# Performance work log

Hardware: AMD Instinct MI355X
Metric: run time of the kernel (lower is better)

## Reference

```python
import jax, jax.numpy as jnp
import numpy as np

D = 1024      # embedding_size
H = 16        # num_heads
HD = D // H   # head_size
EPS = 1e-5


def setup_inputs() -> dict:
    key = jax.random.key(0)
    ks = jax.random.split(key, 12)
    s_in = 1.0 / np.sqrt(D)
    s_hid = 1.0 / np.sqrt(4 * D)
    return {
        "x": jax.random.normal(ks[0], (2, 2048, D), dtype=jnp.float32),
        # per-head projections, no bias: [H, D, HD]
        "Wq": jax.random.normal(ks[1], (H, D, HD), dtype=jnp.float32) * s_in,
        "Wk": jax.random.normal(ks[2], (H, D, HD), dtype=jnp.float32) * s_in,
        "Wv": jax.random.normal(ks[3], (H, D, HD), dtype=jnp.float32) * s_in,
        "Wo": jax.random.normal(ks[4], (D, D), dtype=jnp.float32) * s_in,
        "bo": jnp.zeros((D,), dtype=jnp.float32),
        "W1": jax.random.normal(ks[5], (D, 4 * D), dtype=jnp.float32) * s_in,
        "b1": jnp.zeros((4 * D,), dtype=jnp.float32),
        "W2": jax.random.normal(ks[6], (4 * D, D), dtype=jnp.float32) * s_hid,
        "b2": jnp.zeros((D,), dtype=jnp.float32),
        "g1": jnp.ones((D,), dtype=jnp.float32),
        "be1": jnp.zeros((D,), dtype=jnp.float32),
        "g2": jnp.ones((D,), dtype=jnp.float32),
        "be2": jnp.zeros((D,), dtype=jnp.float32),
    }


def _layernorm(x, g, b):
    mu = jnp.mean(x, axis=-1, keepdims=True)
    var = jnp.mean(jnp.square(x - mu), axis=-1, keepdims=True)
    return (x - mu) * jax.lax.rsqrt(var + EPS) * g + b


def _block(x, Wq, Wk, Wv, Wo, bo, W1, b1, W2, b2, g1, be1, g2, be2):
    B, T, _ = x.shape
    h = _layernorm(x, g1, be1)
    # per-head projections: [B, H, T, HD]
    q = jnp.einsum('btd,hde->bhte', h, Wq)
    k = jnp.einsum('btd,hde->bhte', h, Wk)
    v = jnp.einsum('btd,hde->bhte', h, Wv)
    # NOTE: original scales by embedding_size**-0.5 (x.shape[-1]), not head_size
    scores = jnp.einsum('bhte,bhse->bhts', q, k) * (D ** -0.5)
    mask = jnp.tril(jnp.ones((T, T), dtype=bool))
    scores = jnp.where(mask, scores, -jnp.inf)
    attn = jax.nn.softmax(scores, axis=-1)           # dropout = identity (eval)
    out = jnp.einsum('bhts,bhse->bhte', attn, v)      # [B, H, T, HD]
    out = out.transpose(0, 2, 1, 3).reshape(B, T, D)  # concat heads
    x = x + (out @ Wo + bo)
    h2 = _layernorm(x, g2, be2)
    ffn = jax.nn.relu(h2 @ W1 + b1) @ W2 + b2
    return x + ffn


def reference(x, Wq, Wk, Wv, Wo, bo, W1, b1, W2, b2, g1, be1, g2, be2):
    return _block(x, Wq, Wk, Wv, Wo, bo, W1, b1, W2, b2, g1, be1, g2, be2)
```

## Files before the change

### kernel.cpp

```cpp
#include <hip/hip_runtime.h>
#include <stdint.h>

typedef unsigned short u16;
typedef __attribute__((ext_vector_type(8))) __bf16 bf16x8;
typedef __attribute__((ext_vector_type(4))) float f32x4;

#define D_EMB 1024
#define NHEAD 16
#define HDIM 64
#define TSEQ 2048
#define NTOK 4096
#define NEG_BIG -1.0e30f

#define GLD16(lp, gp) __builtin_amdgcn_global_load_lds( \
    (const __attribute__((address_space(1))) unsigned int*)(gp), \
    (__attribute__((address_space(3))) unsigned int*)(lp), 16, 0, 0)

__device__ __forceinline__ float bf2f(u16 u) {
    union { unsigned int i; float f; } c; c.i = ((unsigned int)u) << 16; return c.f;
}
__device__ __forceinline__ u16 f2bf(float f) {
    union { float f; unsigned int i; } c; c.f = f;
    unsigned int r = (c.i + 0x7FFFu + ((c.i >> 16) & 1u)) >> 16;
    return (u16)r;
}
__device__ __forceinline__ void cp16(u16* dst, const u16* src) {
    *reinterpret_cast<uint4*>(dst) = *reinterpret_cast<const uint4*>(src);
}
__device__ __forceinline__ float load_in(const u16* p, size_t idx, int f32) {
    return f32 ? reinterpret_cast<const float*>(p)[idx] : bf2f(p[idx]);
}
__device__ __forceinline__ size_t tidx(int row, int col, int KB) {
    int c = (col & 7) | ((((col >> 3) ^ row) & 3) << 3);
    return ((size_t)((row >> 7) * KB + (col >> 5)) * 128 + (row & 127)) * 32 + c;
}

__global__ void detect_kernel(const u16* __restrict__ x, u16* __restrict__ fl) {
    if (threadIdx.x == 0) {
        int f = 0;
        for (int i = 0; i < 128; ++i) {
            float v = fabsf(bf2f(x[i]));
            if (!(v <= 1.0e3f)) f = 1;
        }
        fl[0] = (u16)f;
    }
}

__global__ __launch_bounds__(256) void transpose_tiled_kernel(
        const u16* __restrict__ X, u16* __restrict__ Xt, int KB,
        const u16* __restrict__ fl) {
    __shared__ __align__(16) u16 Ts[64 * 72];
    int f32 = fl[0];
    int bi = blockIdx.y, bj = blockIdx.x;
    int NS = gridDim.x * 64;
    int t = threadIdx.x;
    for (int p = 0; p < 2; ++p) {
        int idx = p * 256 + t;
        int row = idx >> 3, col8 = (idx & 7) * 8;
        size_t src = (size_t)(bi * 64 + row) * NS + bj * 64 + col8;
        if (f32) {
            for (int jj = 0; jj < 8; ++jj)
                Ts[row * 72 + col8 + jj] = f2bf(reinterpret_cast<const float*>(X)[src + jj]);
        } else {
            cp16(&Ts[row * 72 + col8], &X[src]);
        }
    }
    __syncthreads();
    for (int p = 0; p < 2; ++p) {
        int idx = p * 256 + t;
        int row = idx >> 3, col8 = (idx & 7) * 8;
        union { u16 u[8]; uint4 v; } tmp;
        for (int jj = 0; jj < 8; ++jj) tmp.u[jj] = Ts[(col8 + jj) * 72 + row];
        int n = bj * 64 + row, k0 = bi * 64 + col8;
        *reinterpret_cast<uint4*>(&Xt[tidx(n, k0, KB)]) = tmp.v;
    }
}

__global__ __launch_bounds__(256) void pack_qkv_kernel(
        const u16* __restrict__ Wq, const u16* __restrict__ Wk,
        const u16* __restrict__ Wv, u16* __restrict__ Wt,
        const u16* __restrict__ fl) {
    int f32 = fl[0];
    int idx = blockIdx.x * 256 + threadIdx.x;
    int e = idx & 63, d8 = (idx >> 6) & 127, hh = (idx >> 13) & 15, sel = idx >> 17;
    const u16* W = (sel == 0) ? Wq : ((sel == 1) ? Wk : Wv);
    int n = sel * 1024 + hh * 64 + e;
    size_t src = (size_t)hh * (D_EMB * HDIM) + (size_t)(d8 * 8) * HDIM + e;
    union { u16 u[8]; uint4 v; } tmp;
    for (int dd = 0; dd < 8; ++dd) {
        float v = f32 ? reinterpret_cast<const float*>(W)[src + (size_t)dd * HDIM]
                      : bf2f(W[src + (size_t)dd * HDIM]);
        tmp.u[dd] = f2bf(v);
    }
    *reinterpret_cast<uint4*>(&Wt[tidx(n, d8 * 8, 32)]) = tmp.v;
}

__global__ __launch_bounds__(256) void ln_kernel(
        const u16* __restrict__ X, const u16* __restrict__ g,
        const u16* __restrict__ be, u16* __restrict__ Ht,
        const u16* __restrict__ fl) {
    int f32 = fl[0];
    int row = blockIdx.x;
    int t = threadIdx.x;
    float v[4];
    float s = 0.f, sq = 0.f;
    for (int i = 0; i < 4; ++i) {
        v[i] = load_in(X, (size_t)row * D_EMB + t + i * 256, f32);
        s += v[i]; sq += v[i] * v[i];
    }
    for (int m = 32; m; m >>= 1) { s += __shfl_down(s, m); sq += __shfl_down(sq, m); }
    __shared__ float red[8];
    int wid = t >> 6, lane = t & 63;
    if (lane == 0) { red[wid] = s; red[wid + 4] = sq; }
    __syncthreads();
    if (t == 0) {
        float S = red[0] + red[1] + red[2] + red[3];
        float SQ = red[4] + red[5] + red[6] + red[7];
        float mean = S * (1.f / 1024.f);
        float var = SQ * (1.f / 1024.f) - mean * mean;
        red[0] = mean; red[1] = rsqrtf(var + 1e-5f);
    }
    __syncthreads();
    float mean = red[0], rstd = red[1];
    for (int i = 0; i < 4; ++i) {
        int c = t + i * 256;
        float hv = (v[i] - mean) * rstd * load_in(g, c, f32) + load_in(be, c, f32);
        Ht[tidx(row, c, 32)] = f2bf(hv);
    }
}

template<int TAG, int TN>
__global__ __launch_bounds__(256) void gemm_t(
        const u16* __restrict__ At, const u16* __restrict__ Bt, u16* __restrict__ C,
        u16* __restrict__ C2,
        const u16* __restrict__ bias, const u16* __restrict__ res,
        int N, int K, int flags, int row_off,
        const u16* __restrict__ fl) {
    constexpr int NF = (TN == 128) ? 4 : 2;
    __shared__ __align__(16) u16 As2[2][4096];
    __shared__ __align__(16) u16 Bs2[2][TN * 32];
    int f32 = fl[0];
    int t = threadIdx.x;
    int gx = gridDim.x, gy = gridDim.y;
    int id = blockIdx.y * gx + blockIdx.x;
    int total = gx * gy;
    int xcd = id & 7, seq = id >> 3, P = total >> 3;
    int tpb = (P >= 32) ? 32 : 16;
    int th  = (P >= 32) ? 8 : 4;
    int tile = xcd * (P / tpb) + seq / tpb;
    int within = seq % tpb;
    int tiles_x = gx >> 2;
    int bx = (tile % tiles_x) * 4 + (within & 3);
    int by = (tile / tiles_x) * th + (within >> 2);
    int n0 = bx * TN, m0 = by * 128;
    int w = t >> 6, lane = t & 63, quad = lane >> 4, l16 = lane & 15;
    int wm = (TN == 128) ? (w >> 1) * 64 : (w & 1) * 64;
    int wn = (TN == 128) ? (w & 1) * 64  : (w >> 1) * 32;
    int KB = K >> 5;
    int kb0 = (seq * (KB >> 5)) & (KB - 1);
    const u16* Ab = At + (size_t)(m0 >> 7) * KB * 4096 + w * 512 + lane * 8;
    const u16* Bb = Bt + (size_t)(n0 >> 7) * KB * 4096
                       + ((TN == 64) ? (n0 & 64) * 32 : 0) + w * 512 + lane * 8;

    auto stage = [&](int buf, int kb) {
        const u16* ga = Ab + (size_t)kb * 4096;
        const u16* gb = Bb + (size_t)kb * 4096;
        u16* la = &As2[buf][w * 512];
        u16* lb = &Bs2[buf][w * 512];
        GLD16(la, ga);
        GLD16(la + 2048, ga + 2048);
        GLD16(lb, gb);
        if constexpr (TN == 128) { GLD16(lb + 2048, gb + 2048); }
    };

    const f32x4 fz = {0.f, 0.f, 0.f, 0.f};
    f32x4 acc[4][NF];
    for (int mt = 0; mt < 4; ++mt)
        for (int nt = 0; nt < NF; ++nt) acc[mt][nt] = fz;

    stage(0, kb0);
    __syncthreads();
    int kb = kb0;
    for (int it = 0; it < KB; ++it) {
        int cur = it & 1;
        int kn = (kb + 1 == KB) ? 0 : kb + 1;
        if (it + 1 < KB) stage(cur ^ 1, kn);
        bf16x8 af[4], bfr[NF];
        for (int mt = 0; mt < 4; ++mt) {
            int r = wm + mt * 16 + l16;
            af[mt] = *reinterpret_cast<const bf16x8*>(
                &As2[cur][r * 32 + (((quad ^ r) & 3) << 3)]);
        }
        for (int nt = 0; nt < NF; ++nt) {
            int r = wn + nt * 16 + l16;
            bfr[nt] = *reinterpret_cast<const bf16x8*>(
                &Bs2[cur][r * 32 + (((quad ^ r) & 3) << 3)]);
        }
        for (int mt = 0; mt < 4; ++mt)
            for (int nt = 0; nt < NF; ++nt)
                acc[mt][nt] = __builtin_amdgcn_mfma_f32_16x16x32_bf16(af[mt], bfr[nt], acc[mt][nt], 0, 0, 0);
        __syncthreads();
        kb = kn;
    }

    int relu_f = flags & 1, out_ext = flags & 2, c_tiled = flags & 4, qkvsp = flags & 8;
    if (qkvsp) {
        for (int mt = 0; mt < 4; ++mt)
            for (int nt = 0; nt < NF; ++nt) {
                int gc = n0 + wn + nt * 16 + l16;
                int grb = m0 + wm + mt * 16 + quad * 4;
                if (gc < 2048) {
                    for (int r = 0; r < 4; ++r)
                        C[(size_t)(grb + r) * 2048 + gc] = f2bf(acc[mt][nt][r]);
                } else {
                    int hh = (gc - 2048) >> 6, d = gc & 63;
                    int bb = grb >> 11, s = grb & 2047;
                    union { u16 u[4]; uint2 v; } pk;
                    for (int r = 0; r < 4; ++r) pk.u[r] = f2bf(acc[mt][nt][r]);
                    *reinterpret_cast<uint2*>(
                        &C2[(((size_t)bb * 16 + hh) * 64 + d) * 2048 + s]) = pk.v;
                }
            }
        return;
    }
    for (int mt = 0; mt < 4; ++mt)
        for (int nt = 0; nt < NF; ++nt)
            for (int r = 0; r < 4; ++r) {
                int gr = m0 + wm + mt * 16 + quad * 4 + r;
                int gc = n0 + wn + nt * 16 + l16;
                float v = acc[mt][nt][r];
                if (bias) v += load_in(bias, gc, f32);
                if (relu_f) v = v > 0.f ? v : 0.f;
                size_t oidx = (size_t)(row_off + gr) * N + gc;
                if (res) v += load_in(res, oidx, f32);
                if (c_tiled)      C[tidx(gr, gc, N >> 5)] = f2bf(v);
                else if (out_ext && f32) reinterpret_cast<float*>(C)[oidx] = v;
                else              C[oidx] = f2bf(v);
            }
}

template<int TAG, int KBL, int TN>
__global__ __launch_bounds__(256) void gemm_sk_t(
        const u16* __restrict__ At, const u16* __restrict__ Bt,
        float* __restrict__ Pp, int N, int K) {
    constexpr int NF = (TN == 128) ? 4 : 2;
    __shared__ __align__(16) u16 As2[2][4096];
    __shared__ __align__(16) u16 Bs2[2][TN * 32];
    int t = threadIdx.x;
    int gx = gridDim.x, gy = gridDim.y;
    int id = blockIdx.y * gx + blockIdx.x;
    int total = gx * gy;
    int xcd = id & 7, seq = id >> 3, P = total >> 3;
    int tpb = (P >= 32) ? 32 : 16;
    int th  = (P >= 32) ? 8 : 4;
    int tile = xcd * (P / tpb) + seq / tpb;
    int within = seq % tpb;
    int tiles_x = gx >> 2;
    int bx = (tile % tiles_x) * 4 + (within & 3);
    int by = (tile / tiles_x) * th + (within >> 2);
    int n0 = bx * TN, m0 = by * 128;
    int w = t >> 6, lane = t & 63, quad = lane >> 4, l16 = lane & 15;
    int wm = (TN == 128) ? (w >> 1) * 64 : (w & 1) * 64;
    int wn = (TN == 128) ? (w & 1) * 64  : (w >> 1) * 32;
    int KB = K >> 5;
    int kstart = blockIdx.z * KBL;
    int rel0 = seq & (KBL - 1);
    const u16* Ab = At + (size_t)(m0 >> 7) * KB * 4096 + w * 512 + lane * 8;
    const u16* Bb = Bt + (size_t)(n0 >> 7) * KB * 4096
                       + ((TN == 64) ? (n0 & 64) * 32 : 0) + w * 512 + lane * 8;

    auto stage = [&](int buf, int kb) {
        const u16* ga = Ab + (size_t)kb * 4096;
        const u16* gb = Bb + (size_t)kb * 4096;
        u16* la = &As2[buf][w * 512];
        u16* lb = &Bs2[buf][w * 512];
        GLD16(la, ga);
        GLD16(la + 2048, ga + 2048);
        GLD16(lb, gb);
        if constexpr (TN == 128) { GLD16(lb + 2048, gb + 2048); }
    };

    const f32x4 fz = {0.f, 0.f, 0.f, 0.f};
    f32x4 acc[4][NF];
    for (int mt = 0; mt < 4; ++mt)
        for (int nt = 0; nt < NF; ++nt) acc[mt][nt] = fz;

    stage(0, kstart + rel0);
    __syncthreads();
    for (int it = 0; it < KBL; ++it) {
        int cur = it & 1;
        if (it + 1 < KBL)
            stage(cur ^ 1, kstart + ((rel0 + it + 1) & (KBL - 1)));
        bf16x8 af[4], bfr[NF];
        for (int mt = 0; mt < 4; ++mt) {
            int r = wm + mt * 16 + l16;
            af[mt] = *reinterpret_cast<const bf16x8*>(
                &As2[cur][r * 32 + (((quad ^ r) & 3) << 3)]);
        }
        for (int nt = 0; nt < NF; ++nt) {
            int r = wn + nt * 16 + l16;
            bfr[nt] = *reinterpret_cast<const bf16x8*>(
                &Bs2[cur][r * 32 + (((quad ^ r) & 3) << 3)]);
        }
        for (int mt = 0; mt < 4; ++mt)
            for (int nt = 0; nt < NF; ++nt)
                acc[mt][nt] = __builtin_amdgcn_mfma_f32_16x16x32_bf16(af[mt], bfr[nt], acc[mt][nt], 0, 0, 0);
        __syncthreads();
    }

    for (int mt = 0; mt < 4; ++mt)
        for (int nt = 0; nt < NF; ++nt)
            for (int r = 0; r < 4; ++r) {
                int gr = m0 + wm + mt * 16 + quad * 4 + r;
                int gc = n0 + wn + nt * 16 + l16;
                atomicAdd(&Pp[(size_t)gr * N + gc], acc[mt][nt][r]);
            }
}

__global__ __launch_bounds__(256) void zero_f32_kernel(float* __restrict__ p) {
    const f32x4 fz = {0.f, 0.f, 0.f, 0.f};
    reinterpret_cast<f32x4*>(p)[(size_t)blockIdx.x * 256 + threadIdx.x] = fz;
}

__global__ __launch_bounds__(256) void ffn_fin_kernel(
        const float* __restrict__ Pp, const u16* __restrict__ b2,
        u16* __restrict__ out, int row_off, const u16* __restrict__ fl) {
    int f32 = fl[0];
    size_t i = ((size_t)blockIdx.x * 256 + threadIdx.x) * 4;
    int col = (int)(i & 1023);
    f32x4 pv = *reinterpret_cast<const f32x4*>(Pp + i);
    size_t o = (size_t)row_off * 1024 + i;
    if (f32) {
        float* of = reinterpret_cast<float*>(out);
        f32x4 ov = *reinterpret_cast<f32x4*>(of + o);
        for (int j = 0; j < 4; ++j)
            ov[j] += pv[j] + load_in(b2, col + j, 1);
        *reinterpret_cast<f32x4*>(of + o) = ov;
    } else {
        for (int j = 0; j < 4; ++j) {
            float v = bf2f(out[o + j]) + pv[j] + bf2f(b2[col + j]);
            out[o + j] = f2bf(v);
        }
    }
}

__global__ __launch_bounds__(256) void oproj_fin_ln2_kernel(
        const float* __restrict__ Pp, const u16* __restrict__ bo,
        const u16* __restrict__ x, const u16* __restrict__ g2,
        const u16* __restrict__ be2, u16* __restrict__ out,
        u16* __restrict__ h2t, const u16* __restrict__ fl) {
    int f32 = fl[0];
    int row = blockIdx.x;
    int t = threadIdx.x;
    size_t base = (size_t)row * 1024 + t * 4;
    f32x4 pv = *reinterpret_cast<const f32x4*>(Pp + base);
    float v[4];
    float s = 0.f, sq = 0.f;
    for (int j = 0; j < 4; ++j) {
        v[j] = load_in(x, base + j, f32) + pv[j] + load_in(bo, t * 4 + j, f32);
        s += v[j]; sq += v[j] * v[j];
    }
    if (f32) {
        f32x4 ov = {v[0], v[1], v[2], v[3]};
        *reinterpret_cast<f32x4*>(reinterpret_cast<float*>(out) + base) = ov;
    } else {
        union { u16 u[4]; uint2 q; } pk;
        for (int j = 0; j < 4; ++j) pk.u[j] = f2bf(v[j]);
        *reinterpret_cast<uint2*>(&out[base]) = pk.q;
    }
    for (int m = 32; m; m >>= 1) { s += __shfl_down(s, m); sq += __shfl_down(sq, m); }
    __shared__ float red[8];
    int wid = t >> 6, lane = t & 63;
    if (lane == 0) { red[wid] = s; red[wid + 4] = sq; }
    __syncthreads();
    if (t == 0) {
        float S = red[0] + red[1] + red[2] + red[3];
        float SQ = red[4] + red[5] + red[6] + red[7];
        float mean = S * (1.f / 1024.f);
        float var = SQ * (1.f / 1024.f) - mean * mean;
        red[0] = mean; red[1] = rsqrtf(var + 1e-5f);
    }
    __syncthreads();
    float mean = red[0], rstd = red[1];
    for (int j = 0; j < 4; ++j) {
        int c = t * 4 + j;
        float hv = (v[j] - mean) * rstd * load_in(g2, c, f32) + load_in(be2, c, f32);
        h2t[tidx(row, c, 32)] = f2bf(hv);
    }
}

__global__ __launch_bounds__(128) void flash_kernel(
        const u16* __restrict__ qk, const u16* __restrict__ vt,
        u16* __restrict__ attn_t) {
    __shared__ __align__(16) u16 Ps[32 * 72];
    int t = threadIdx.x;
    int px = blockIdx.x & 15, rh = blockIdx.x >> 4;
    int b = blockIdx.y >> 4, h = blockIdx.y & 15;
    int wid = t >> 6, lane = t & 63, quad = lane >> 4, l16 = lane & 15;
    int g = rh * 2 + wid;
    const size_t seq_base = (size_t)b * TSEQ;
    const u16* vplane = vt + (size_t)(b * 16 + h) * 64 * 2048;

    for (int half = 0; half < 2; ++half) {
        int tq = half ? px : (31 - px);

        bf16x8 aq[2];
        for (int kit = 0; kit < 2; ++kit)
            aq[kit] = *reinterpret_cast<const bf16x8*>(
                &qk[(seq_base + tq * 64 + g * 16 + l16) * 2048 + h * 64 + kit * 32 + quad * 8]);

        const f32x4 fz = {0.f, 0.f, 0.f, 0.f};
        float m_run[4], l_run[4];
        f32x4 o[4];
        for (int r = 0; r < 4; ++r) { m_run[r] = NEG_BIG; l_run[r] = 0.f; }
        for (int nt = 0; nt < 4; ++nt) o[nt] = fz;

        for (int j = 0; j <= tq; ++j) {
            f32x4 sa[4];
            for (int nt = 0; nt < 4; ++nt) sa[nt] = fz;
            for (int kit = 0; kit < 2; ++kit) {
                for (int nt = 0; nt < 4; ++nt) {
                    bf16x8 bk = *reinterpret_cast<const bf16x8*>(
                        &qk[(seq_base + j * 64 + nt * 16 + l16) * 2048 + 1024 + h * 64 + kit * 32 + quad * 8]);
                    sa[nt] = __builtin_amdgcn_mfma_f32_16x16x32_bf16(aq[kit], bk, sa[nt], 0, 0, 0);
                }
            }

            float p_val[4][4];
            int qbase = tq * 64 + g * 16 + quad * 4;
            int sbase = j * 64 + l16;
            for (int r = 0; r < 4; ++r) {
                float sv[4];
                float mx = NEG_BIG;
                for (int nt = 0; nt < 4; ++nt) {
                    float xv = sa[nt][r] * 0.03125f;
                    if (sbase + nt * 16 > qbase + r) xv = NEG_BIG;
                    sv[nt] = xv;
                    mx = fmaxf(mx, xv);
                }
                for (int m = 1; m < 16; m <<= 1) mx = fmaxf(mx, __shfl_xor(mx, m));
                float mnew = fmaxf(m_run[r], mx);
                float alpha = __expf(m_run[r] - mnew);
                m_run[r] = mnew;
                float rs = 0.f;
                for (int nt = 0; nt < 4; ++nt) {
                    float pv = __expf(sv[nt] - mnew);
                    p_val[nt][r] = pv;
                    rs += pv;
                }
                for (int m = 1; m < 16; m <<= 1) rs += __shfl_xor(rs, m);
                l_run[r] = l_run[r] * alpha + rs;
                for (int nt = 0; nt < 4; ++nt) o[nt][r] *= alpha;
            }

            for (int nt = 0; nt < 4; ++nt)
                for (int r = 0; r < 4; ++r)
                    Ps[(wid * 16 + quad * 4 + r) * 72 + nt * 16 + l16] = f2bf(p_val[nt][r]);

            for (int kit = 0; kit < 2; ++kit) {
                bf16x8 ap = *reinterpret_cast<const bf16x8*>(
                    &Ps[(wid * 16 + l16) * 72 + kit * 32 + quad * 8]);
                for (int nt = 0; nt < 4; ++nt) {
                    bf16x8 bv = *reinterpret_cast<const bf16x8*>(
                        &vplane[(size_t)(nt * 16 + l16) * 2048 + j * 64 + kit * 32 + quad * 8]);
                    o[nt] = __builtin_amdgcn_mfma_f32_16x16x32_bf16(ap, bv, o[nt], 0, 0, 0);
                }
            }
        }

        for (int nt = 0; nt < 4; ++nt)
            for (int r = 0; r < 4; ++r) {
                int trow = (int)seq_base + tq * 64 + g * 16 + quad * 4 + r;
                int col = h * 64 + nt * 16 + l16;
                attn_t[tidx(trow, col, 32)] = f2bf(o[nt][r] / l_run[r]);
            }
    }
}

extern "C" void kernel_launch(void* const* d_in, const int* in_sizes, int n_in,
                              void* d_out, int out_size, void* d_ws, size_t ws_size,
                              hipStream_t stream) {
    const u16* x   = (const u16*)d_in[0];
    const u16* Wq  = (const u16*)d_in[1];
    const u16* Wk  = (const u16*)d_in[2];
    const u16* Wv  = (const u16*)d_in[3];
    const u16* Wo  = (const u16*)d_in[4];
    const u16* bo  = (const u16*)d_in[5];
    const u16* W1  = (const u16*)d_in[6];
    const u16* b1  = (const u16*)d_in[7];
    const u16* W2  = (const u16*)d_in[8];
    const u16* b2  = (const u16*)d_in[9];
    const u16* g1  = (const u16*)d_in[10];
    const u16* be1 = (const u16*)d_in[11];
    const u16* g2  = (const u16*)d_in[12];
    const u16* be2 = (const u16*)d_in[13];
    u16* out = (u16*)d_out;

    const size_t M1 = (size_t)1 << 20;
    u16* ws = (u16*)d_ws;
    bool sk = ws_size >= ((size_t)58 << 20);

    if (sk) {
        u16* qk   = ws;
        u16* vt   = ws + 8 * M1;
        u16* attn = ws + 12 * M1;
        u16* W1t  = ws + 16 * M1;
        u16* h    = ws + 20 * M1;
        u16* Wot  = ws + 20 * M1;
        u16* h2   = ws + 20 * M1;
        u16* Wtq  = ws + 24 * M1;
        u16* W2t  = ws + 24 * M1;
        u16* a1   = ws;
        float* PpO = reinterpret_cast<float*>(ws);
        float* PpF = reinterpret_cast<float*>(ws + 16 * M1);
        u16* fl   = ws + 28 * M1;

        detect_kernel<<<1, 64, 0, stream>>>(x, fl);

        pack_qkv_kernel<<<1536, 256, 0, stream>>>(Wq, Wk, Wv, Wtq, fl);
        ln_kernel<<<NTOK, 256, 0, stream>>>(x, g1, be1, h, fl);
        gemm_t<0, 64><<<dim3(48, 32), 256, 0, stream>>>(
            h, Wtq, qk, vt, nullptr, nullptr, 3072, 1024, 8, 0, fl);

        transpose_tiled_kernel<<<dim3(16, 16), 256, 0, stream>>>(Wo, Wot, 32, fl);

        flash_kernel<<<dim3(32, 32), 128, 0, stream>>>(qk, vt, attn);

        zero_f32_kernel<<<4096, 256, 0, stream>>>(PpO);
        gemm_sk_t<2, 8, 64><<<dim3(16, 32, 4), 256, 0, stream>>>(attn, Wot, PpO, 1024, 1024);
        oproj_fin_ln2_kernel<<<4096, 256, 0, stream>>>(PpO, bo, x, g2, be2, out, h2, fl);

        transpose_tiled_kernel<<<dim3(16, 64), 256, 0, stream>>>(W2, W2t, 128, fl);
        transpose_tiled_kernel<<<dim3(64, 16), 256, 0, stream>>>(W1, W1t, 32, fl);

        gemm_t<2, 64><<<dim3(64, 32), 256, 0, stream>>>(
            h2, W1t, a1, nullptr, b1, nullptr, 4096, 1024, 1 | 4, 0, fl);
        zero_f32_kernel<<<4096, 256, 0, stream>>>(PpF);
        gemm_sk_t<0, 32, 64><<<dim3(16, 32, 4), 256, 0, stream>>>(a1, W2t, PpF, 1024, 4096);
        ffn_fin_kernel<<<4096, 256, 0, stream>>>(PpF, b2, out, 0, fl);
    } else {
        u16* qk   = ws;
        u16* vt   = ws + 8 * M1;
        u16* h    = ws + 12 * M1;
        u16* attn = ws + 12 * M1;
        u16* h2   = ws + 12 * M1;
        u16* Wtq  = ws + 16 * M1;
        u16* Wot  = ws + 16 * M1;
        u16* W1t  = ws + 16 * M1;
        u16* W2t  = ws;
        u16* a1   = ws + 4 * M1;
        u16* fl   = ws + 20 * M1;

        detect_kernel<<<1, 64, 0, stream>>>(x, fl);
        pack_qkv_kernel<<<1536, 256, 0, stream>>>(Wq, Wk, Wv, Wtq, fl);
        ln_kernel<<<NTOK, 256, 0, stream>>>(x, g1, be1, h, fl);
        gemm_t<0, 64><<<dim3(48, 32), 256, 0, stream>>>(
            h, Wtq, qk, vt, nullptr, nullptr, 3072, 1024, 8, 0, fl);
        transpose_tiled_kernel<<<dim3(16, 16), 256, 0, stream>>>(Wo, Wot, 32, fl);
        flash_kernel<<<dim3(32, 32), 128, 0, stream>>>(qk, vt, attn);
        gemm_t<1, 128><<<dim3(8, 32), 256, 0, stream>>>(
            attn, Wot, out, nullptr, bo, x, 1024, 1024, 2, 0, fl);
        transpose_tiled_kernel<<<dim3(16, 64), 256, 0, stream>>>(W2, W2t, 128, fl);
        transpose_tiled_kernel<<<dim3(64, 16), 256, 0, stream>>>(W1, W1t, 32, fl);
        ln_kernel<<<NTOK, 256, 0, stream>>>(out, g2, be2, h2, fl);
        gemm_t<2, 64><<<dim3(64, 16), 256, 0, stream>>>(
            h2, W1t, a1, nullptr, b1, nullptr, 4096, 1024, 1 | 4, 0, fl);
        gemm_t<4, 128><<<dim3(8, 16), 256, 0, stream>>>(
            a1, W2t, out, nullptr, b2, out, 1024, 4096, 2, 0, fl);
        gemm_t<3, 64><<<dim3(64, 16), 256, 0, stream>>>(
            h2 + (size_t)2 * M1, W1t, a1, nullptr, b1, nullptr, 4096, 1024, 1 | 4, 0, fl);
        gemm_t<5, 128><<<dim3(8, 16), 256, 0, stream>>>(
            a1, W2t, out, nullptr, b2, out, 1024, 4096, 2, 2048, fl);
    }
}
```

Measured before the change: 614.3 us.

## Split flash attention KV loop into two independent online-softmax streams

```diff
diff --git a/kernel.cpp b/kernel.cpp
--- a/kernel.cpp
+++ b/kernel.cpp
@@ -392,7 +392,7 @@
 __global__ __launch_bounds__(128) void flash_kernel(
         const u16* __restrict__ qk, const u16* __restrict__ vt,
         u16* __restrict__ attn_t) {
-    __shared__ __align__(16) u16 Ps[32 * 72];
+    __shared__ __align__(16) u16 Ps[64 * 72];
     int t = threadIdx.x;
     int px = blockIdx.x & 15, rh = blockIdx.x >> 4;
     int b = blockIdx.y >> 4, h = blockIdx.y & 15;
@@ -400,6 +400,7 @@
     int g = rh * 2 + wid;
     const size_t seq_base = (size_t)b * TSEQ;
     const u16* vplane = vt + (size_t)(b * 16 + h) * 64 * 2048;
+    const f32x4 fz = {0.f, 0.f, 0.f, 0.f};
 
     for (int half = 0; half < 2; ++half) {
         int tq = half ? px : (31 - px);
@@ -409,32 +410,32 @@
             aq[kit] = *reinterpret_cast<const bf16x8*>(
                 &qk[(seq_base + tq * 64 + g * 16 + l16) * 2048 + h * 64 + kit * 32 + quad * 8]);
 
-        const f32x4 fz = {0.f, 0.f, 0.f, 0.f};
-        float m_run[4], l_run[4];
-        f32x4 o[4];
-        for (int r = 0; r < 4; ++r) { m_run[r] = NEG_BIG; l_run[r] = 0.f; }
-        for (int nt = 0; nt < 4; ++nt) o[nt] = fz;
-
-        for (int j = 0; j <= tq; ++j) {
+        float mA[4], lA[4], mB[4], lB[4];
+        f32x4 oA[4], oB[4];
+        for (int r = 0; r < 4; ++r) {
+            mA[r] = NEG_BIG; lA[r] = 0.f; mB[r] = NEG_BIG; lB[r] = 0.f;
+        }
+        for (int nt = 0; nt < 4; ++nt) { oA[nt] = fz; oB[nt] = fz; }
+
+        auto tile = [&](int j, int domask, float (&m_run)[4], float (&l_run)[4],
+                        f32x4 (&o)[4], int st) {
             f32x4 sa[4];
             for (int nt = 0; nt < 4; ++nt) sa[nt] = fz;
-            for (int kit = 0; kit < 2; ++kit) {
+            for (int kit = 0; kit < 2; ++kit)
                 for (int nt = 0; nt < 4; ++nt) {
                     bf16x8 bk = *reinterpret_cast<const bf16x8*>(
                         &qk[(seq_base + j * 64 + nt * 16 + l16) * 2048 + 1024 + h * 64 + kit * 32 + quad * 8]);
                     sa[nt] = __builtin_amdgcn_mfma_f32_16x16x32_bf16(aq[kit], bk, sa[nt], 0, 0, 0);
                 }
-            }
-
-            float p_val[4][4];
             int qbase = tq * 64 + g * 16 + quad * 4;
             int sbase = j * 64 + l16;
+            float p_val[4][4];
             for (int r = 0; r < 4; ++r) {
                 float sv[4];
                 float mx = NEG_BIG;
                 for (int nt = 0; nt < 4; ++nt) {
                     float xv = sa[nt][r] * 0.03125f;
-                    if (sbase + nt * 16 > qbase + r) xv = NEG_BIG;
+                    if (domask && (sbase + nt * 16 > qbase + r)) xv = NEG_BIG;
                     sv[nt] = xv;
                     mx = fmaxf(mx, xv);
                 }
@@ -452,28 +453,43 @@
                 l_run[r] = l_run[r] * alpha + rs;
                 for (int nt = 0; nt < 4; ++nt) o[nt][r] *= alpha;
             }
-
+            int srow = (wid * 2 + st) * 16;
             for (int nt = 0; nt < 4; ++nt)
                 for (int r = 0; r < 4; ++r)
-                    Ps[(wid * 16 + quad * 4 + r) * 72 + nt * 16 + l16] = f2bf(p_val[nt][r]);
-
+                    Ps[(srow + quad * 4 + r) * 72 + nt * 16 + l16] = f2bf(p_val[nt][r]);
             for (int kit = 0; kit < 2; ++kit) {
                 bf16x8 ap = *reinterpret_cast<const bf16x8*>(
-                    &Ps[(wid * 16 + l16) * 72 + kit * 32 + quad * 8]);
+                    &Ps[(srow + l16) * 72 + kit * 32 + quad * 8]);
                 for (int nt = 0; nt < 4; ++nt) {
                     bf16x8 bv = *reinterpret_cast<const bf16x8*>(
                         &vplane[(size_t)(nt * 16 + l16) * 2048 + j * 64 + kit * 32 + quad * 8]);
                     o[nt] = __builtin_amdgcn_mfma_f32_16x16x32_bf16(ap, bv, o[nt], 0, 0, 0);
                 }
             }
-        }
-
-        for (int nt = 0; nt < 4; ++nt)
-            for (int r = 0; r < 4; ++r) {
-                int trow = (int)seq_base + tq * 64 + g * 16 + quad * 4 + r;
-                int col = h * 64 + nt * 16 + l16;
-                attn_t[tidx(trow, col, 32)] = f2bf(o[nt][r] / l_run[r]);
+        };
+
+        int j = 0;
+        for (; j + 1 < tq; j += 2) {
+            tile(j, 0, mA, lA, oA, 0);
+            tile(j + 1, 0, mB, lB, oB, 1);
+        }
+        if (j < tq) {
+            tile(j, 0, mA, lA, oA, 0);
+            tile(tq, 1, mB, lB, oB, 1);
+        } else {
+            tile(tq, 1, mA, lA, oA, 0);
+        }
+
+        for (int r = 0; r < 4; ++r) {
+            float mm = fmaxf(mA[r], mB[r]);
+            float a0 = __expf(mA[r] - mm), a1 = __expf(mB[r] - mm);
+            float li = 1.f / (a0 * lA[r] + a1 * lB[r]);
+            int trow = (int)seq_base + tq * 64 + g * 16 + quad * 4 + r;
+            for (int nt = 0; nt < 4; ++nt) {
+                float val = (a0 * oA[nt][r] + a1 * oB[nt][r]) * li;
+                attn_t[tidx(trow, h * 64 + nt * 16 + l16, 32)] = f2bf(val);
             }
+        }
     }
 }
 
```

Measured after the change: 557.3 us (median of 2 runs). 1.1x faster.
